# Performance work log

Hardware: AMD Instinct MI355X
Metric: run time of the kernel (lower is better)

## Reference

```python
import jax, jax.numpy as jnp
import numpy as np

EPS = 1e-5
NUM_GROUPS = 32
NUM_HEADS = 4


def setup_inputs() -> dict:
    key = jax.random.key(0)
    ks = jax.random.split(key, 7)
    b, c, h, w = 4, 256, 64, 64
    x = jax.random.normal(ks[0], (b, c, h, w), dtype=jnp.float32)
    gn_w = jax.random.normal(ks[1], (c,), dtype=jnp.float32) * 0.02 + 1.0
    gn_b = jax.random.normal(ks[2], (c,), dtype=jnp.float32) * 0.02
    qkv_w = jax.random.normal(ks[3], (3 * c, c), dtype=jnp.float32) * (1.0 / np.sqrt(c))
    qkv_b = jax.random.normal(ks[4], (3 * c,), dtype=jnp.float32) * 0.02
    proj_w = jax.random.normal(ks[5], (c, c), dtype=jnp.float32) * (1.0 / np.sqrt(c))
    proj_b = jax.random.normal(ks[6], (c,), dtype=jnp.float32) * 0.02
    return {"x": x, "gn_w": gn_w, "gn_b": gn_b, "qkv_w": qkv_w,
            "qkv_b": qkv_b, "proj_w": proj_w, "proj_b": proj_b}


def _group_norm(x, w, b):
    # GroupNorm32: compute in float32, cast back to input dtype
    bsz, c, h, ww = x.shape
    xf = x.astype(jnp.float32).reshape(bsz, NUM_GROUPS, c // NUM_GROUPS, h, ww)
    mean = xf.mean(axis=(2, 3, 4), keepdims=True)
    var = xf.var(axis=(2, 3, 4), keepdims=True)
    xn = (xf - mean) * jax.lax.rsqrt(var + EPS)
    xn = xn.reshape(bsz, c, h, ww)
    xn = xn * w[None, :, None, None] + b[None, :, None, None]
    return xn.astype(x.dtype)


def reference(x, gn_w, gn_b, qkv_w, qkv_b, proj_w, proj_b):
    b, c, h, w = x.shape
    hd = c // NUM_HEADS
    n = h * w
    xn = _group_norm(x, gn_w, gn_b)
    # 1x1 conv == per-pixel linear: [b, 3c, h, w]
    qkv = jnp.einsum('oc,bchw->bohw', qkv_w, xn) + qkv_b[None, :, None, None]
    qkv = qkv.reshape(b, 3, NUM_HEADS, hd, n)
    q, k, v = qkv[:, 0], qkv[:, 1], qkv[:, 2]  # [b, H, hd, n]
    scale = hd ** -0.5
    # scores [b, H, n, n]
    attn = jnp.einsum('bhdq,bhdk->bhqk', q, k) * scale
    attn = jax.nn.softmax(attn, axis=-1)
    out = jnp.einsum('bhqk,bhdk->bhdq', attn, v)  # [b, H, hd, n]
    out = out.reshape(b, c, h, w)
    out = jnp.einsum('oc,bchw->bohw', proj_w, out) + proj_b[None, :, None, None]
    return x + out
```

## Files before the change

### kernel.cpp

```cpp
#include <hip/hip_runtime.h>

typedef __attribute__((ext_vector_type(8))) short bfrag;
typedef __attribute__((ext_vector_type(4))) float ffrag;
typedef __attribute__((ext_vector_type(8))) unsigned short us8;
typedef __attribute__((ext_vector_type(4))) unsigned short us4;
typedef __attribute__((ext_vector_type(2))) unsigned short us2;

#define DEVI static __device__ __forceinline__

DEVI unsigned short f2bf(float f){
  unsigned int u = __float_as_uint(f);
  u += 0x7fffu + ((u >> 16) & 1u);
  return (unsigned short)(u >> 16);
}
DEVI float fexp2(float x){ float r; asm("v_exp_f32 %0, %1" : "=v"(r) : "v"(x)); return r; }
DEVI unsigned int cvt_pk_bf16(float lo, float hi){
  unsigned int r;
  asm("v_cvt_pk_bf16_f32 %0, %1, %2" : "=v"(r) : "v"(lo), "v"(hi));
  return r;
}
DEVI int swz64(int r, int c){ return ((r << 6) + c) ^ ((r & 7) << 3); }
DEVI int swz256(int r, int c){ return ((r << 8) + c) ^ ((r & 7) << 3); }

DEVI void gload16(const unsigned short* g, unsigned short* l){
  __builtin_amdgcn_global_load_lds(
      (const __attribute__((address_space(1))) unsigned int*)g,
      (__attribute__((address_space(3))) unsigned int*)l, 16, 0, 0);
}

__global__ __launch_bounds__(256) void prep_gn(
    const float* __restrict__ x, const float* __restrict__ gw,
    const float* __restrict__ gb, const float* __restrict__ qkvw,
    const float* __restrict__ qkvb, const float* __restrict__ pw,
    unsigned short* __restrict__ wq, unsigned short* __restrict__ wp,
    float* __restrict__ bq, unsigned short* __restrict__ xnt){
  __shared__ float ps[4], pq[4];
  if (blockIdx.x >= 128){
    const int i = (blockIdx.x - 128) * 256 + threadIdx.x;
    const float qs = 0.125f * 1.44269504f;
    if (i < 49152){
      float4 v = ((const float4*)qkvw)[i];
      float sc = (i < 16384) ? qs : 1.f;
      us4 u; u[0]=f2bf(v.x*sc); u[1]=f2bf(v.y*sc); u[2]=f2bf(v.z*sc); u[3]=f2bf(v.w*sc);
      ((us4*)wq)[i] = u;
    }
    if (i < 16384){
      float4 v = ((const float4*)pw)[i];
      us4 u; u[0]=f2bf(v.x); u[1]=f2bf(v.y); u[2]=f2bf(v.z); u[3]=f2bf(v.w);
      ((us4*)wp)[i] = u;
    }
    if (i < 768) bq[i] = qkvb[i] * (i < 256 ? qs : 1.f);
    return;
  }
  const int b = blockIdx.x >> 5, g = blockIdx.x & 31;
  const int t = threadIdx.x;
  const float* xb = x + (((size_t)b * 256 + g * 8) << 12);
  float s = 0.f, q = 0.f;
  #pragma unroll
  for (int c = 0; c < 8; ++c){
    const float4* base = (const float4*)(xb + ((size_t)c << 12));
    #pragma unroll
    for (int e = 0; e < 4; ++e){
      float4 v = base[e * 256 + t];
      s += v.x + v.y + v.z + v.w;
      q += v.x * v.x + v.y * v.y + v.z * v.z + v.w * v.w;
    }
  }
  #pragma unroll
  for (int m = 32; m; m >>= 1){ s += __shfl_down(s, m); q += __shfl_down(q, m); }
  if ((t & 63) == 0){ ps[t >> 6] = s; pq[t >> 6] = q; }
  __syncthreads();
  float S = ps[0] + ps[1] + ps[2] + ps[3];
  float Q = pq[0] + pq[1] + pq[2] + pq[3];
  float mean = S * (1.f / 32768.f);
  float var  = Q * (1.f / 32768.f) - mean * mean;
  float rstd = rsqrtf(var + 1e-5f);
  float sc[8], sh[8];
  #pragma unroll
  for (int c = 0; c < 8; ++c){
    sc[c] = gw[g * 8 + c] * rstd;
    sh[c] = gb[g * 8 + c] - mean * sc[c];
  }
  unsigned short* dst = xnt + (((size_t)b << 12) << 8) + (g << 3);
  #pragma unroll
  for (int e = 0; e < 16; ++e){
    const int n = e * 256 + t;
    us8 u;
    #pragma unroll
    for (int c = 0; c < 8; ++c)
      u[c] = f2bf(xb[((size_t)c << 12) + n] * sc[c] + sh[c]);
    *(us8*)(dst + ((size_t)n << 8)) = u;
  }
}

__global__ __launch_bounds__(256) void qkv_gemm(
    const unsigned short* __restrict__ xnt, const unsigned short* __restrict__ W,
    const float* __restrict__ bias, unsigned short* __restrict__ qt,
    unsigned short* __restrict__ kt, unsigned short* __restrict__ vt){
  const int n0 = blockIdx.x << 6, MT = blockIdx.y, b = blockIdx.z;
  const int t = threadIdx.x, l = t & 63, w = t >> 6;
  __shared__ __align__(16) unsigned short AB[32768];
  unsigned short* Al = AB;
  unsigned short* Bl = AB + 16384;
  const unsigned short* Asrc = W + (size_t)(MT << 6) * 256;
  const unsigned short* Bsrc = xnt + ((((size_t)b << 12) + n0) << 8);
  #pragma unroll
  for (int e = 0; e < 8; ++e){
    const int idx = e * 256 + t;
    const int r = idx >> 5, g = idx & 31;
    const int gs = (g ^ (r & 7)) << 3;
    unsigned short* db = &AB[(e * 256 + (w << 6)) << 3];
    gload16(Asrc + (r << 8) + gs, db);
    gload16(Bsrc + (r << 8) + gs, db + 16384);
  }
  __syncthreads();
  ffrag acc[4] = {{0,0,0,0},{0,0,0,0},{0,0,0,0},{0,0,0,0}};
  #pragma unroll
  for (int kc = 0; kc < 8; ++kc){
    bfrag a = *(const bfrag*)&Al[swz256((w << 4) + (l & 15), (kc << 5) + ((l >> 4) << 3))];
    #pragma unroll
    for (int fc = 0; fc < 4; ++fc){
      bfrag bb = *(const bfrag*)&Bl[swz256((fc << 4) + (l & 15), (kc << 5) + ((l >> 4) << 3))];
      acc[fc] = __builtin_amdgcn_mfma_f32_16x16x32_bf16(a, bb, acc[fc], 0, 0, 0);
    }
  }
  const int which = MT >> 2, h = MT & 3;
  const int d0 = (w << 4) + ((l >> 4) << 2);
  float bi[4];
  #pragma unroll
  for (int r = 0; r < 4; ++r) bi[r] = bias[(MT << 6) + d0 + r];
  #pragma unroll
  for (int fc = 0; fc < 4; ++fc){
    int n = n0 + (fc << 4) + (l & 15);
    if (which < 2){
      unsigned short* dst = (which == 0 ? qt : kt) +
          (((size_t)(b * 4 + h)) << 18) + ((size_t)n << 6) + d0;
      us4 u;
      #pragma unroll
      for (int r = 0; r < 4; ++r) u[r] = f2bf(acc[fc][r] + bi[r]);
      *(us4*)dst = u;
    } else {
      const int np = n0 + ((fc & 2) << 4) + (((l >> 2) & 3) << 3)
                        + ((fc & 1) << 2) + (l & 3);
      #pragma unroll
      for (int r = 0; r < 4; ++r)
        vt[((((size_t)(b * 4 + h)) << 6) + d0 + r) * 4096 + np] = f2bf(acc[fc][r] + bi[r]);
    }
  }
}

__global__ __launch_bounds__(512, 4) void attn_kernel(
    const unsigned short* __restrict__ qt, const unsigned short* __restrict__ kt,
    const unsigned short* __restrict__ vt, unsigned short* __restrict__ at){
  const int id = blockIdx.x;
  const int xc = id & 7, k2 = id >> 3;
  const int bhid = (xc << 1) + (k2 >> 5);
  const int qx = k2 & 31;
  const int b = bhid >> 2, h = bhid & 3;
  const int q0 = qx << 7;
  const int t = threadIdx.x, l = t & 63, w = t >> 6;
  const int wq = w & 3, kh = w >> 2;
  const size_t bh = (size_t)bhid;
  __shared__ __align__(16) unsigned short S[32768];
  const unsigned short* kbase = kt + (bh << 18);
  const unsigned short* vbase = vt + (bh << 18);

  const int row = t >> 3;
  const int gx = ((t & 7) ^ (row & 7)) << 3;
  const int koff = (row << 6) + gx;
  unsigned short* ldst = &S[w << 9];
  const unsigned short* qsrc = qt + (bh << 18) + ((size_t)q0 << 6);
  gload16(qsrc + koff, ldst + 8192);
  gload16(qsrc + 4096 + koff, ldst + 12288);
  gload16(kbase + koff, ldst);
  gload16(vbase + (row << 12) + gx, ldst + 16384);
  gload16(kbase + 4096 + koff, ldst + 4096);
  gload16(vbase + (row << 12) + 64 + gx, ldst + 20480);
  asm volatile("s_waitcnt vmcnt(4)" ::: "memory");
  __builtin_amdgcn_s_barrier();
  __builtin_amdgcn_sched_barrier(0);
  const int qreg = (wq >> 1) ? 12288 : 8192;
  const int qrow = ((wq & 1) << 5) + (l & 15);
  bfrag bq00 = *(const bfrag*)&S[qreg + swz64(qrow,      (l >> 4) << 3)];
  bfrag bq01 = *(const bfrag*)&S[qreg + swz64(qrow, 32 + ((l >> 4) << 3))];
  bfrag bq10 = *(const bfrag*)&S[qreg + swz64(qrow + 16,      (l >> 4) << 3)];
  bfrag bq11 = *(const bfrag*)&S[qreg + swz64(qrow + 16, 32 + ((l >> 4) << 3))];
  asm volatile("s_waitcnt lgkmcnt(0)" ::: "memory");
  asm volatile("s_waitcnt vmcnt(2)" ::: "memory");
  __builtin_amdgcn_s_barrier();
  __builtin_amdgcn_sched_barrier(0);

  ffrag acc[2][4] = {{{0,0,0,0},{0,0,0,0},{0,0,0,0},{0,0,0,0}},
                     {{0,0,0,0},{0,0,0,0},{0,0,0,0},{0,0,0,0}}};
  ffrag zs[2] = {{0,0,0,0},{0,0,0,0}};
  const ffrag zf = {0.f, 0.f, 0.f, 0.f};
  bfrag onesB;
  #pragma unroll
  for (int j = 0; j < 8; ++j) onesB[j] = (short)0x3F80;

  auto body = [&](int kbr, int vbr) __attribute__((always_inline)) {
    ffrag s[2][2];
    __builtin_amdgcn_s_setprio(1);
    #pragma unroll
    for (int j = 0; j < 2; ++j){
      const int fc = (kh << 1) + j;
      bfrag ak0 = *(const bfrag*)&S[kbr + swz64((fc << 4) + (l & 15), (l >> 4) << 3)];
      bfrag ak1 = *(const bfrag*)&S[kbr + swz64((fc << 4) + (l & 15), 32 + ((l >> 4) << 3))];
      ffrag z0 = __builtin_amdgcn_mfma_f32_16x16x32_bf16(ak0, bq00, zf, 0, 0, 0);
      z0 = __builtin_amdgcn_mfma_f32_16x16x32_bf16(ak1, bq01, z0, 0, 0, 0);
      ffrag z1 = __builtin_amdgcn_mfma_f32_16x16x32_bf16(ak0, bq10, zf, 0, 0, 0);
      z1 = __builtin_amdgcn_mfma_f32_16x16x32_bf16(ak1, bq11, z1, 0, 0, 0);
      s[0][j] = z0; s[1][j] = z1;
    }
    __builtin_amdgcn_s_setprio(0);
    float p[2][2][4];
    #pragma unroll
    for (int g = 0; g < 2; ++g){
      #pragma unroll
      for (int j = 0; j < 2; ++j){
        #pragma unroll
        for (int r = 0; r < 4; ++r) p[g][j][r] = fexp2(s[g][j][r]);
      }
    }
    union { bfrag bb; unsigned int u[4]; } A0, A1;
    A0.u[0] = cvt_pk_bf16(p[0][0][0], p[0][0][1]); A0.u[1] = cvt_pk_bf16(p[0][0][2], p[0][0][3]);
    A0.u[2] = cvt_pk_bf16(p[0][1][0], p[0][1][1]); A0.u[3] = cvt_pk_bf16(p[0][1][2], p[0][1][3]);
    A1.u[0] = cvt_pk_bf16(p[1][0][0], p[1][0][1]); A1.u[1] = cvt_pk_bf16(p[1][0][2], p[1][0][3]);
    A1.u[2] = cvt_pk_bf16(p[1][1][0], p[1][1][1]); A1.u[3] = cvt_pk_bf16(p[1][1][2], p[1][1][3]);
    __builtin_amdgcn_s_setprio(1);
    zs[0] = __builtin_amdgcn_mfma_f32_16x16x32_bf16(A0.bb, onesB, zs[0], 0, 0, 0);
    zs[1] = __builtin_amdgcn_mfma_f32_16x16x32_bf16(A1.bb, onesB, zs[1], 0, 0, 0);
    #pragma unroll
    for (int fc = 0; fc < 4; ++fc){
      bfrag vv = *(const bfrag*)&S[vbr + swz64((fc << 4) + (l & 15),
                                              (kh << 5) + ((l >> 4) << 3))];
      acc[0][fc] = __builtin_amdgcn_mfma_f32_16x16x32_bf16(A0.bb, vv, acc[0][fc], 0, 0, 0);
      acc[1][fc] = __builtin_amdgcn_mfma_f32_16x16x32_bf16(A1.bb, vv, acc[1][fc], 0, 0, 0);
    }
    __builtin_amdgcn_s_setprio(0);
  };
  auto issue2 = [&](int kti2, int buf) __attribute__((always_inline)) {
    gload16(kbase + (kti2 << 12) + koff, ldst + (buf << 12));
    gload16(vbase + (row << 12) + (kti2 << 6) + gx, ldst + 16384 + (buf << 12));
  };

#define ATTN_PAIR(KE, BE, BO)                                 \
    issue2((KE) + 2, ((BE) + 2) & 3);                         \
    body((BE) << 12, 16384 + ((BE) << 12));                   \
    asm volatile("s_waitcnt vmcnt(2)" ::: "memory");          \
    __builtin_amdgcn_sched_barrier(0);                        \
    issue2((KE) + 3, ((BO) + 2) & 3);                         \
    body((BO) << 12, 16384 + ((BO) << 12));                   \
    asm volatile("s_waitcnt vmcnt(2)" ::: "memory");          \
    __builtin_amdgcn_s_barrier();                             \
    __builtin_amdgcn_sched_barrier(0);

  for (int base = 0; base < 60; base += 4){
    ATTN_PAIR(base + 0, 0, 1)
    ATTN_PAIR(base + 2, 2, 3)
  }
  ATTN_PAIR(60, 0, 1)
  body(2 << 12, 16384 + (2 << 12));
  asm volatile("s_waitcnt vmcnt(0)" ::: "memory");
  __builtin_amdgcn_sched_barrier(0);
  body(3 << 12, 16384 + (3 << 12));
#undef ATTN_PAIR

  __syncthreads();
  float* Sf = (float*)S;
  if (kh == 1 && (l & 15) == 0){
    #pragma unroll
    for (int g = 0; g < 2; ++g){
      #pragma unroll
      for (int r = 0; r < 4; ++r)
        Sf[8192 + (wq << 5) + (g << 4) + ((l >> 4) << 2) + r] = zs[g][r];
    }
  }
  __syncthreads();
  float inv[2][4];
  if (kh == 0){
    #pragma unroll
    for (int g = 0; g < 2; ++g){
      #pragma unroll
      for (int r = 0; r < 4; ++r)
        inv[g][r] = 1.f / (zs[g][r] +
            Sf[8192 + (wq << 5) + (g << 4) + ((l >> 4) << 2) + r]);
    }
  }
  __syncthreads();
  if (kh == 1){
    #pragma unroll
    for (int g = 0; g < 2; ++g){
      #pragma unroll
      for (int fc = 0; fc < 4; ++fc){
        #pragma unroll
        for (int r = 0; r < 4; ++r)
          Sf[((wq << 5) + (g << 4) + ((l >> 4) << 2) + r) * 64 + (fc << 4) + (l & 15)] =
              acc[g][fc][r];
      }
    }
  }
  __syncthreads();
  if (kh == 0){
    #pragma unroll
    for (int g = 0; g < 2; ++g){
      #pragma unroll
      for (int fc = 0; fc < 4; ++fc){
        #pragma unroll
        for (int r = 0; r < 4; ++r){
          const int ql = (wq << 5) + (g << 4) + ((l >> 4) << 2) + r;
          float ob = Sf[ql * 64 + (fc << 4) + (l & 15)];
          float v = (acc[g][fc][r] + ob) * inv[g][r];
          at[((((size_t)b << 12) + q0 + ql) << 8) + (h << 6) + (fc << 4) + (l & 15)] =
              f2bf(v);
        }
      }
    }
  }
}

__global__ __launch_bounds__(256) void proj_gemm(
    const unsigned short* __restrict__ at, const unsigned short* __restrict__ W,
    const float* __restrict__ bias, const float* __restrict__ x,
    float* __restrict__ out){
  const int n0 = blockIdx.x << 6, MT = blockIdx.y, b = blockIdx.z;
  const int t = threadIdx.x, l = t & 63, w = t >> 6;
  __shared__ __align__(16) unsigned short AB[32768];
  unsigned short* Al = AB;
  unsigned short* Bl = AB + 16384;
  const unsigned short* Asrc = W + (size_t)(MT << 6) * 256;
  const unsigned short* Bsrc = at + ((((size_t)b << 12) + n0) << 8);
  #pragma unroll
  for (int e = 0; e < 8; ++e){
    const int idx = e * 256 + t;
    const int r = idx >> 5, g = idx & 31;
    const int gs = (g ^ (r & 7)) << 3;
    unsigned short* db = &AB[(e * 256 + (w << 6)) << 3];
    gload16(Asrc + (r << 8) + gs, db);
    gload16(Bsrc + (r << 8) + gs, db + 16384);
  }
  __syncthreads();
  ffrag acc[4] = {{0,0,0,0},{0,0,0,0},{0,0,0,0},{0,0,0,0}};
  #pragma unroll
  for (int kc = 0; kc < 8; ++kc){
    bfrag a = *(const bfrag*)&Al[swz256((w << 4) + (l & 15), (kc << 5) + ((l >> 4) << 3))];
    #pragma unroll
    for (int fc = 0; fc < 4; ++fc){
      bfrag bb = *(const bfrag*)&Bl[swz256((fc << 4) + (l & 15), (kc << 5) + ((l >> 4) << 3))];
      acc[fc] = __builtin_amdgcn_mfma_f32_16x16x32_bf16(a, bb, acc[fc], 0, 0, 0);
    }
  }
  const int co = (MT << 6) + (w << 4) + ((l >> 4) << 2);
  #pragma unroll
  for (int fc = 0; fc < 4; ++fc){
    int n = n0 + (fc << 4) + (l & 15);
    #pragma unroll
    for (int r = 0; r < 4; ++r){
      size_t o = (((size_t)b * 256 + co + r) << 12) + n;
      out[o] = acc[fc][r] + bias[co + r] + x[o];
    }
  }
}

extern "C" void kernel_launch(void* const* d_in, const int* in_sizes, int n_in,
                              void* d_out, int out_size, void* d_ws, size_t ws_size,
                              hipStream_t stream){
  const float* x    = (const float*)d_in[0];
  const float* gw   = (const float*)d_in[1];
  const float* gb   = (const float*)d_in[2];
  const float* qkvw = (const float*)d_in[3];
  const float* qkvb = (const float*)d_in[4];
  const float* pw   = (const float*)d_in[5];
  const float* pb   = (const float*)d_in[6];
  float* out = (float*)d_out;

  unsigned short* xnt = (unsigned short*)((char*)d_ws + 16384);
  unsigned short* qt  = xnt + (size_t)4 * 4096 * 256;
  unsigned short* kt  = qt  + (size_t)16 * 4096 * 64;
  unsigned short* vt  = kt  + (size_t)16 * 4096 * 64;
  unsigned short* at  = vt  + (size_t)16 * 4096 * 64;
  unsigned short* wq  = at  + (size_t)4 * 4096 * 256;
  unsigned short* wp  = wq  + (size_t)768 * 256;
  float*          bq  = (float*)(wp + (size_t)256 * 256);

  prep_gn    <<<384, 256, 0, stream>>>(x, gw, gb, qkvw, qkvb, pw, wq, wp, bq, xnt);
  qkv_gemm   <<<dim3(64, 12, 4), 256, 0, stream>>>(xnt, wq, bq, qt, kt, vt);
  attn_kernel<<<dim3(512), 512, 0, stream>>>(qt, kt, vt, at);
  proj_gemm  <<<dim3(64, 4, 4), 256, 0, stream>>>(at, wp, pb, x, out);
}
```

Before: 113.5 us.

## Halve attention query tile to 64 rows with double-buffered K/V and more blocks

The attention kernel now handles 64 query rows per block instead of 128, doubling the grid to 1024 blocks. Shared memory drops to 32KB, the K/V ring shrinks from four stages to two, and the launch-bounds occupancy hint rises from 4 to 6. The goal is more resident blocks and fewer registers per thread so latency is hidden better. The cost is that each K/V tile is reused by half as many queries, which doubles K/V global traffic. The prefetch is also shallower, with a full vmcnt(0) wait and a barrier on every tile.

```diff
diff --git a/kernel.cpp b/kernel.cpp
--- a/kernel.cpp
+++ b/kernel.cpp
@@ -149,19 +149,19 @@
   }
 }
 
-__global__ __launch_bounds__(512, 4) void attn_kernel(
+__global__ __launch_bounds__(512, 6) void attn_kernel(
     const unsigned short* __restrict__ qt, const unsigned short* __restrict__ kt,
     const unsigned short* __restrict__ vt, unsigned short* __restrict__ at){
   const int id = blockIdx.x;
   const int xc = id & 7, k2 = id >> 3;
-  const int bhid = (xc << 1) + (k2 >> 5);
-  const int qx = k2 & 31;
+  const int bhid = (xc << 1) + (k2 >> 6);
+  const int qx = k2 & 63;
   const int b = bhid >> 2, h = bhid & 3;
-  const int q0 = qx << 7;
+  const int q0 = qx << 6;
   const int t = threadIdx.x, l = t & 63, w = t >> 6;
   const int wq = w & 3, kh = w >> 2;
   const size_t bh = (size_t)bhid;
-  __shared__ __align__(16) unsigned short S[32768];
+  __shared__ __align__(16) unsigned short S[16384];
   const unsigned short* kbase = kt + (bh << 18);
   const unsigned short* vbase = vt + (bh << 18);
 
@@ -170,150 +170,120 @@
   const int koff = (row << 6) + gx;
   unsigned short* ldst = &S[w << 9];
   const unsigned short* qsrc = qt + (bh << 18) + ((size_t)q0 << 6);
-  gload16(qsrc + koff, ldst + 8192);
-  gload16(qsrc + 4096 + koff, ldst + 12288);
+  gload16(qsrc + koff, ldst + 4096);
   gload16(kbase + koff, ldst);
-  gload16(vbase + (row << 12) + gx, ldst + 16384);
-  gload16(kbase + 4096 + koff, ldst + 4096);
-  gload16(vbase + (row << 12) + 64 + gx, ldst + 20480);
-  asm volatile("s_waitcnt vmcnt(4)" ::: "memory");
-  __builtin_amdgcn_s_barrier();
-  __builtin_amdgcn_sched_barrier(0);
-  const int qreg = (wq >> 1) ? 12288 : 8192;
-  const int qrow = ((wq & 1) << 5) + (l & 15);
-  bfrag bq00 = *(const bfrag*)&S[qreg + swz64(qrow,      (l >> 4) << 3)];
-  bfrag bq01 = *(const bfrag*)&S[qreg + swz64(qrow, 32 + ((l >> 4) << 3))];
-  bfrag bq10 = *(const bfrag*)&S[qreg + swz64(qrow + 16,      (l >> 4) << 3)];
-  bfrag bq11 = *(const bfrag*)&S[qreg + swz64(qrow + 16, 32 + ((l >> 4) << 3))];
-  asm volatile("s_waitcnt lgkmcnt(0)" ::: "memory");
+  gload16(vbase + (row << 12) + gx, ldst + 8192);
   asm volatile("s_waitcnt vmcnt(2)" ::: "memory");
   __builtin_amdgcn_s_barrier();
   __builtin_amdgcn_sched_barrier(0);
-
-  ffrag acc[2][4] = {{{0,0,0,0},{0,0,0,0},{0,0,0,0},{0,0,0,0}},
-                     {{0,0,0,0},{0,0,0,0},{0,0,0,0},{0,0,0,0}}};
-  ffrag zs[2] = {{0,0,0,0},{0,0,0,0}};
+  bfrag bq0 = *(const bfrag*)&S[4096 + swz64((wq << 4) + (l & 15), (l >> 4) << 3)];
+  bfrag bq1 = *(const bfrag*)&S[4096 + swz64((wq << 4) + (l & 15), 32 + ((l >> 4) << 3))];
+  asm volatile("s_waitcnt lgkmcnt(0)" ::: "memory");
+  __builtin_amdgcn_s_barrier();
+  __builtin_amdgcn_sched_barrier(0);
+  gload16(kbase + 4096 + koff, ldst + 4096);
+  gload16(vbase + (row << 12) + 64 + gx, ldst + 12288);
+  asm volatile("s_waitcnt vmcnt(2)" ::: "memory");
+  __builtin_amdgcn_s_barrier();
+  __builtin_amdgcn_sched_barrier(0);
+
+  ffrag acc[4] = {{0,0,0,0},{0,0,0,0},{0,0,0,0},{0,0,0,0}};
+  ffrag zs = {0,0,0,0};
   const ffrag zf = {0.f, 0.f, 0.f, 0.f};
   bfrag onesB;
   #pragma unroll
   for (int j = 0; j < 8; ++j) onesB[j] = (short)0x3F80;
 
   auto body = [&](int kbr, int vbr) __attribute__((always_inline)) {
-    ffrag s[2][2];
+    ffrag s[2];
     __builtin_amdgcn_s_setprio(1);
     #pragma unroll
     for (int j = 0; j < 2; ++j){
       const int fc = (kh << 1) + j;
       bfrag ak0 = *(const bfrag*)&S[kbr + swz64((fc << 4) + (l & 15), (l >> 4) << 3)];
       bfrag ak1 = *(const bfrag*)&S[kbr + swz64((fc << 4) + (l & 15), 32 + ((l >> 4) << 3))];
-      ffrag z0 = __builtin_amdgcn_mfma_f32_16x16x32_bf16(ak0, bq00, zf, 0, 0, 0);
-      z0 = __builtin_amdgcn_mfma_f32_16x16x32_bf16(ak1, bq01, z0, 0, 0, 0);
-      ffrag z1 = __builtin_amdgcn_mfma_f32_16x16x32_bf16(ak0, bq10, zf, 0, 0, 0);
-      z1 = __builtin_amdgcn_mfma_f32_16x16x32_bf16(ak1, bq11, z1, 0, 0, 0);
-      s[0][j] = z0; s[1][j] = z1;
+      ffrag z = __builtin_amdgcn_mfma_f32_16x16x32_bf16(ak0, bq0, zf, 0, 0, 0);
+      z = __builtin_amdgcn_mfma_f32_16x16x32_bf16(ak1, bq1, z, 0, 0, 0);
+      s[j] = z;
     }
     __builtin_amdgcn_s_setprio(0);
-    float p[2][2][4];
-    #pragma unroll
-    for (int g = 0; g < 2; ++g){
-      #pragma unroll
-      for (int j = 0; j < 2; ++j){
-        #pragma unroll
-        for (int r = 0; r < 4; ++r) p[g][j][r] = fexp2(s[g][j][r]);
-      }
-    }
-    union { bfrag bb; unsigned int u[4]; } A0, A1;
-    A0.u[0] = cvt_pk_bf16(p[0][0][0], p[0][0][1]); A0.u[1] = cvt_pk_bf16(p[0][0][2], p[0][0][3]);
-    A0.u[2] = cvt_pk_bf16(p[0][1][0], p[0][1][1]); A0.u[3] = cvt_pk_bf16(p[0][1][2], p[0][1][3]);
-    A1.u[0] = cvt_pk_bf16(p[1][0][0], p[1][0][1]); A1.u[1] = cvt_pk_bf16(p[1][0][2], p[1][0][3]);
-    A1.u[2] = cvt_pk_bf16(p[1][1][0], p[1][1][1]); A1.u[3] = cvt_pk_bf16(p[1][1][2], p[1][1][3]);
+    float p[2][4];
+    #pragma unroll
+    for (int j = 0; j < 2; ++j){
+      #pragma unroll
+      for (int r = 0; r < 4; ++r) p[j][r] = fexp2(s[j][r]);
+    }
+    union { bfrag bb; unsigned int u[4]; } A;
+    A.u[0] = cvt_pk_bf16(p[0][0], p[0][1]); A.u[1] = cvt_pk_bf16(p[0][2], p[0][3]);
+    A.u[2] = cvt_pk_bf16(p[1][0], p[1][1]); A.u[3] = cvt_pk_bf16(p[1][2], p[1][3]);
     __builtin_amdgcn_s_setprio(1);
-    zs[0] = __builtin_amdgcn_mfma_f32_16x16x32_bf16(A0.bb, onesB, zs[0], 0, 0, 0);
-    zs[1] = __builtin_amdgcn_mfma_f32_16x16x32_bf16(A1.bb, onesB, zs[1], 0, 0, 0);
+    zs = __builtin_amdgcn_mfma_f32_16x16x32_bf16(A.bb, onesB, zs, 0, 0, 0);
     #pragma unroll
     for (int fc = 0; fc < 4; ++fc){
       bfrag vv = *(const bfrag*)&S[vbr + swz64((fc << 4) + (l & 15),
                                               (kh << 5) + ((l >> 4) << 3))];
-      acc[0][fc] = __builtin_amdgcn_mfma_f32_16x16x32_bf16(A0.bb, vv, acc[0][fc], 0, 0, 0);
-      acc[1][fc] = __builtin_amdgcn_mfma_f32_16x16x32_bf16(A1.bb, vv, acc[1][fc], 0, 0, 0);
+      acc[fc] = __builtin_amdgcn_mfma_f32_16x16x32_bf16(A.bb, vv, acc[fc], 0, 0, 0);
     }
     __builtin_amdgcn_s_setprio(0);
   };
   auto issue2 = [&](int kti2, int buf) __attribute__((always_inline)) {
     gload16(kbase + (kti2 << 12) + koff, ldst + (buf << 12));
-    gload16(vbase + (row << 12) + (kti2 << 6) + gx, ldst + 16384 + (buf << 12));
+    gload16(vbase + (row << 12) + (kti2 << 6) + gx, ldst + 8192 + (buf << 12));
   };
 
-#define ATTN_PAIR(KE, BE, BO)                                 \
-    issue2((KE) + 2, ((BE) + 2) & 3);                         \
-    body((BE) << 12, 16384 + ((BE) << 12));                   \
-    asm volatile("s_waitcnt vmcnt(2)" ::: "memory");          \
-    __builtin_amdgcn_sched_barrier(0);                        \
-    issue2((KE) + 3, ((BO) + 2) & 3);                         \
-    body((BO) << 12, 16384 + ((BO) << 12));                   \
-    asm volatile("s_waitcnt vmcnt(2)" ::: "memory");          \
-    __builtin_amdgcn_s_barrier();                             \
+  body(0, 8192);
+  asm volatile("s_waitcnt vmcnt(0)" ::: "memory");
+  __builtin_amdgcn_s_barrier();
+  __builtin_amdgcn_sched_barrier(0);
+  for (int e = 1; e < 63; e += 2){
+    issue2(e + 1, 0);
+    body(1 << 12, 8192 + (1 << 12));
+    asm volatile("s_waitcnt vmcnt(0)" ::: "memory");
+    __builtin_amdgcn_s_barrier();
     __builtin_amdgcn_sched_barrier(0);
-
-  for (int base = 0; base < 60; base += 4){
-    ATTN_PAIR(base + 0, 0, 1)
-    ATTN_PAIR(base + 2, 2, 3)
-  }
-  ATTN_PAIR(60, 0, 1)
-  body(2 << 12, 16384 + (2 << 12));
-  asm volatile("s_waitcnt vmcnt(0)" ::: "memory");
-  __builtin_amdgcn_sched_barrier(0);
-  body(3 << 12, 16384 + (3 << 12));
-#undef ATTN_PAIR
+    if (e + 2 < 64) issue2(e + 2, 1);
+    body(0, 8192);
+    asm volatile("s_waitcnt vmcnt(0)" ::: "memory");
+    __builtin_amdgcn_s_barrier();
+    __builtin_amdgcn_sched_barrier(0);
+  }
+  body(1 << 12, 8192 + (1 << 12));
 
   __syncthreads();
   float* Sf = (float*)S;
   if (kh == 1 && (l & 15) == 0){
     #pragma unroll
-    for (int g = 0; g < 2; ++g){
+    for (int r = 0; r < 4; ++r)
+      Sf[4096 + (wq << 4) + ((l >> 4) << 2) + r] = zs[r];
+  }
+  __syncthreads();
+  float inv[4];
+  if (kh == 0){
+    #pragma unroll
+    for (int r = 0; r < 4; ++r)
+      inv[r] = 1.f / (zs[r] + Sf[4096 + (wq << 4) + ((l >> 4) << 2) + r]);
+  }
+  __syncthreads();
+  if (kh == 1){
+    #pragma unroll
+    for (int fc = 0; fc < 4; ++fc){
       #pragma unroll
       for (int r = 0; r < 4; ++r)
-        Sf[8192 + (wq << 5) + (g << 4) + ((l >> 4) << 2) + r] = zs[g][r];
-    }
-  }
-  __syncthreads();
-  float inv[2][4];
+        Sf[((wq << 4) + ((l >> 4) << 2) + r) * 64 + (fc << 4) + (l & 15)] =
+            acc[fc][r];
+    }
+  }
+  __syncthreads();
   if (kh == 0){
     #pragma unroll
-    for (int g = 0; g < 2; ++g){
-      #pragma unroll
-      for (int r = 0; r < 4; ++r)
-        inv[g][r] = 1.f / (zs[g][r] +
-            Sf[8192 + (wq << 5) + (g << 4) + ((l >> 4) << 2) + r]);
-    }
-  }
-  __syncthreads();
-  if (kh == 1){
-    #pragma unroll
-    for (int g = 0; g < 2; ++g){
-      #pragma unroll
-      for (int fc = 0; fc < 4; ++fc){
-        #pragma unroll
-        for (int r = 0; r < 4; ++r)
-          Sf[((wq << 5) + (g << 4) + ((l >> 4) << 2) + r) * 64 + (fc << 4) + (l & 15)] =
-              acc[g][fc][r];
-      }
-    }
-  }
-  __syncthreads();
-  if (kh == 0){
-    #pragma unroll
-    for (int g = 0; g < 2; ++g){
-      #pragma unroll
-      for (int fc = 0; fc < 4; ++fc){
-        #pragma unroll
-        for (int r = 0; r < 4; ++r){
-          const int ql = (wq << 5) + (g << 4) + ((l >> 4) << 2) + r;
-          float ob = Sf[ql * 64 + (fc << 4) + (l & 15)];
-          float v = (acc[g][fc][r] + ob) * inv[g][r];
-          at[((((size_t)b << 12) + q0 + ql) << 8) + (h << 6) + (fc << 4) + (l & 15)] =
-              f2bf(v);
-        }
+    for (int fc = 0; fc < 4; ++fc){
+      #pragma unroll
+      for (int r = 0; r < 4; ++r){
+        const int ql = (wq << 4) + ((l >> 4) << 2) + r;
+        float ob = Sf[ql * 64 + (fc << 4) + (l & 15)];
+        float v = (acc[fc][r] + ob) * inv[r];
+        at[((((size_t)b << 12) + q0 + ql) << 8) + (h << 6) + (fc << 4) + (l & 15)] =
+            f2bf(v);
       }
     }
   }
@@ -385,6 +355,6 @@
 
   prep_gn    <<<384, 256, 0, stream>>>(x, gw, gb, qkvw, qkvb, pw, wq, wp, bq, xnt);
   qkv_gemm   <<<dim3(64, 12, 4), 256, 0, stream>>>(xnt, wq, bq, qt, kt, vt);
-  attn_kernel<<<dim3(512), 512, 0, stream>>>(qt, kt, vt, at);
+  attn_kernel<<<dim3(1024), 512, 0, stream>>>(qt, kt, vt, at);
   proj_gemm  <<<dim3(64, 4, 4), 256, 0, stream>>>(at, wp, pb, x, out);
 }
```

Result: slower. 129.7 us (+14.3%).
